# Kernel tuning notes

Measured on AMD Instinct MI355X. Metric: run time of the kernel, lower is better.

## Reference

```python
import jax, jax.numpy as jnp
import numpy as np

EPS = 0.01
MAX_ITER = 100


def setup_inputs() -> dict:
    key = jax.random.key(0)
    B, N = 8, 2048
    c = jax.random.normal(key, (B, N, N), dtype=jnp.float32)
    return {"c": c}


def reference(c):
    # Torch code sets C = -c, then M = (-C + u_i + v_j)/eps = (c + u_i + v_j)/eps.
    eps = EPS
    B, n, _ = c.shape
    log_mu = -jnp.log(jnp.asarray(n, c.dtype))  # log(1/n); mu == nu == uniform
    u = jnp.zeros((B, n), c.dtype)
    v = jnp.zeros((B, n), c.dtype)

    def M(u, v):
        return (c + u[:, :, None] + v[:, None, :]) / eps  # [B, n, n]

    @jax.checkpoint
    def step(carry, _):
        u, v = carry
        # even iteration: u update
        u = eps * (log_mu - jax.nn.logsumexp(M(u, v), axis=-1)) + u
        # odd iteration: v update (logsumexp over transpose == axis -2), then
        # detach + clamp of huge values to 0, as in the torch code
        v_new = eps * (log_mu - jax.nn.logsumexp(M(u, v), axis=-2)) + v
        v_new = jnp.where(v_new > 9e8, jnp.zeros_like(v_new), v_new)
        v = jax.lax.stop_gradient(v_new)
        return (u, v), None

    # 100 torch iterations alternate u/v -> 50 fused (u,v) steps.
    # (Early-break threshold is 1e-12 and essentially never triggers; we run
    #  the fixed max_iter count.)
    (u, v), _ = jax.lax.scan(step, (u, v), None, length=MAX_ITER // 2)

    pi = jnp.exp(M(u, v))
    return pi, -c, u, v
```

## Files before the change

### kernel.cpp

```cpp
#include <hip/hip_runtime.h>

#define NN 2048
#define BB 8
#define NITER 50
#define RCHUNKS 16
#define ROWS_PER_CHUNK (NN / RCHUNKS)

__device__ __forceinline__ float eps_f()      { return 0.01f; }
__device__ __forceinline__ float inv_eps_f()  { return 100.0f; }
__device__ __forceinline__ float eps_logmu_f(){ return -0.0762461898616f; }

__device__ __forceinline__ void lse_combine(float& m, float& s, float om, float os) {
    float M = fmaxf(m, om);
    s = s * __expf((m - M) * inv_eps_f()) + os * __expf((om - M) * inv_eps_f());
    m = M;
}

__global__ __launch_bounds__(256) void k_init(float* __restrict__ u, float* __restrict__ v) {
    int idx = blockIdx.x * 256 + threadIdx.x;
    if (idx < BB * NN) { u[idx] = 0.0f; v[idx] = 0.0f; }
}

__global__ __launch_bounds__(256) void k_u(const float* __restrict__ c,
                                           const float* __restrict__ v,
                                           float* __restrict__ u) {
    int row = blockIdx.x;
    int b   = row >> 11;
    int t   = threadIdx.x;
    const float4* crow = (const float4*)(c + (size_t)row * NN);
    const float4* vb   = (const float4*)(v + (size_t)b * NN);

    float4 c0 = crow[t];
    float4 c1 = crow[t + 256];
    float4 v0 = vb[t];
    float4 v1 = vb[t + 256];

    float x[8] = { c0.x + v0.x, c0.y + v0.y, c0.z + v0.z, c0.w + v0.w,
                   c1.x + v1.x, c1.y + v1.y, c1.z + v1.z, c1.w + v1.w };

    float m = x[0];
#pragma unroll
    for (int k = 1; k < 8; ++k) m = fmaxf(m, x[k]);
    float s = 0.0f;
#pragma unroll
    for (int k = 0; k < 8; ++k) s += __expf((x[k] - m) * inv_eps_f());

#pragma unroll
    for (int off = 32; off; off >>= 1) {
        float om = __shfl_xor(m, off, 64);
        float os = __shfl_xor(s, off, 64);
        lse_combine(m, s, om, os);
    }
    __shared__ float sm[4], ss[4];
    int wid = t >> 6;
    if ((t & 63) == 0) { sm[wid] = m; ss[wid] = s; }
    __syncthreads();
    if (t == 0) {
#pragma unroll
        for (int w = 1; w < 4; ++w) lse_combine(m, s, sm[w], ss[w]);
        u[row] = eps_logmu_f() - m - eps_f() * __logf(s);
    }
}

__global__ __launch_bounds__(256) void k_v_partial(const float* __restrict__ c,
                                                   const float* __restrict__ u,
                                                   float* __restrict__ pm,
                                                   float* __restrict__ ps) {
    int j     = blockIdx.x * 256 + threadIdx.x;
    int chunk = blockIdx.y;
    int b     = blockIdx.z;
    const float* cb = c + (size_t)b * NN * NN;
    const float* ub = u + (size_t)b * NN;

    int i0 = chunk * ROWS_PER_CHUNK;
    float m = -INFINITY, s = 0.0f;
    for (int i = i0; i < i0 + ROWS_PER_CHUNK; i += 4) {
        float u0 = ub[i], u1 = ub[i + 1], u2 = ub[i + 2], u3 = ub[i + 3];
        float x0 = cb[(size_t)(i + 0) * NN + j] + u0;
        float x1 = cb[(size_t)(i + 1) * NN + j] + u1;
        float x2 = cb[(size_t)(i + 2) * NN + j] + u2;
        float x3 = cb[(size_t)(i + 3) * NN + j] + u3;
        float lm = fmaxf(fmaxf(x0, x1), fmaxf(x2, x3));
        float ls = __expf((x0 - lm) * inv_eps_f()) + __expf((x1 - lm) * inv_eps_f())
                 + __expf((x2 - lm) * inv_eps_f()) + __expf((x3 - lm) * inv_eps_f());
        lse_combine(m, s, lm, ls);
    }
    int o = (b * RCHUNKS + chunk) * NN + j;
    pm[o] = m;
    ps[o] = s;
}

__global__ __launch_bounds__(256) void k_v_combine(const float* __restrict__ pm,
                                                   const float* __restrict__ ps,
                                                   float* __restrict__ v) {
    int idx = blockIdx.x * 256 + threadIdx.x;
    int b = idx >> 11;
    int j = idx & (NN - 1);
    float m = -INFINITY, s = 0.0f;
#pragma unroll
    for (int r = 0; r < RCHUNKS; ++r) {
        int o = (b * RCHUNKS + r) * NN + j;
        lse_combine(m, s, pm[o], ps[o]);
    }
    float val = eps_logmu_f() - m - eps_f() * __logf(s);
    if (val > 9e8f) val = 0.0f;
    v[idx] = val;
}

__global__ __launch_bounds__(256) void k_final(const float* __restrict__ c,
                                               const float* __restrict__ u,
                                               const float* __restrict__ v,
                                               float* __restrict__ pi,
                                               float* __restrict__ negc) {
    unsigned q = blockIdx.x * 256 + threadIdx.x;
    unsigned e = q * 4;
    unsigned b = e >> 22;
    unsigned rem = e & (NN * NN - 1);
    unsigned i = rem >> 11;
    unsigned j = rem & (NN - 1);

    float4 cc = ((const float4*)c)[q];
    float ui = u[b * NN + i];
    const float* vp = v + b * NN + j;
    float4 vv = *(const float4*)vp;

    float4 p;
    p.x = __expf((cc.x + ui + vv.x) * inv_eps_f());
    p.y = __expf((cc.y + ui + vv.y) * inv_eps_f());
    p.z = __expf((cc.z + ui + vv.z) * inv_eps_f());
    p.w = __expf((cc.w + ui + vv.w) * inv_eps_f());
    ((float4*)pi)[q] = p;

    float4 nc = { -cc.x, -cc.y, -cc.z, -cc.w };
    ((float4*)negc)[q] = nc;
}

__global__ __launch_bounds__(256) void k_uv_out(const float* __restrict__ u,
                                                const float* __restrict__ v,
                                                float* __restrict__ ou,
                                                float* __restrict__ ov) {
    int idx = blockIdx.x * 256 + threadIdx.x;
    if (idx < BB * NN) { ou[idx] = u[idx]; ov[idx] = v[idx]; }
}

extern "C" void kernel_launch(void* const* d_in, const int* in_sizes, int n_in,
                              void* d_out, int out_size, void* d_ws, size_t ws_size,
                              hipStream_t stream) {
    const float* c = (const float*)d_in[0];
    float* out  = (float*)d_out;
    float* pi   = out;
    float* negc = out + (size_t)BB * NN * NN;
    float* ou   = out + 2 * (size_t)BB * NN * NN;
    float* ov   = ou + BB * NN;

    float* ws = (float*)d_ws;
    float* u  = ws;
    float* v  = ws + BB * NN;
    float* pm = ws + 2 * BB * NN;
    float* ps = pm + BB * RCHUNKS * NN;

    k_init<<<(BB * NN) / 256, 256, 0, stream>>>(u, v);

    dim3 gB(NN / 256, RCHUNKS, BB);
    for (int it = 0; it < NITER; ++it) {
        k_u<<<BB * NN, 256, 0, stream>>>(c, v, u);
        k_v_partial<<<gB, 256, 0, stream>>>(c, u, pm, ps);
        k_v_combine<<<(BB * NN) / 256, 256, 0, stream>>>(pm, ps, v);
    }

    unsigned n4 = (unsigned)((size_t)BB * NN * NN / 4);
    k_final<<<n4 / 256, 256, 0, stream>>>(c, u, v, pi, negc);
    k_uv_out<<<(BB * NN) / 256, 256, 0, stream>>>(u, v, ou, ov);
}
```

Before: 2.563 ms.

## Fuse u-update and partial column logsumexp into one pass over c

Merges the row logsumexp (u update) and the column partial logsumexp (v partials) into a single kernel. Each wave loads a row of c once, computes u for that row, then folds the same registers into per-column running max/sum accumulators. This halves the reads of the 128 MB cost matrix per iteration. In exchange it uses only 512 blocks with heavy register and LDS use, and the v combine step now reads 64 partial bands instead of 16.

```diff
diff --git a/kernel.cpp b/kernel.cpp
--- a/kernel.cpp
+++ b/kernel.cpp
@@ -3,8 +3,9 @@
 #define NN 2048
 #define BB 8
 #define NITER 50
-#define RCHUNKS 16
-#define ROWS_PER_CHUNK (NN / RCHUNKS)
+#define NBAND 64
+#define ROWS_PER_WAVE 8
+#define WPB 4
 
 __device__ __forceinline__ float eps_f()      { return 0.01f; }
 __device__ __forceinline__ float inv_eps_f()  { return 100.0f; }
@@ -16,78 +17,107 @@
     m = M;
 }
 
-__global__ __launch_bounds__(256) void k_init(float* __restrict__ u, float* __restrict__ v) {
+__device__ __forceinline__ void colacc(float& m, float& s, float x) {
+    float M = fmaxf(m, x);
+    s = s * __expf((m - M) * inv_eps_f()) + __expf((x - M) * inv_eps_f());
+    m = M;
+}
+
+__global__ __launch_bounds__(256) void k_init(float* __restrict__ v) {
     int idx = blockIdx.x * 256 + threadIdx.x;
-    if (idx < BB * NN) { u[idx] = 0.0f; v[idx] = 0.0f; }
-}
-
-__global__ __launch_bounds__(256) void k_u(const float* __restrict__ c,
-                                           const float* __restrict__ v,
-                                           float* __restrict__ u) {
-    int row = blockIdx.x;
-    int b   = row >> 11;
-    int t   = threadIdx.x;
-    const float4* crow = (const float4*)(c + (size_t)row * NN);
-    const float4* vb   = (const float4*)(v + (size_t)b * NN);
-
-    float4 c0 = crow[t];
-    float4 c1 = crow[t + 256];
-    float4 v0 = vb[t];
-    float4 v1 = vb[t + 256];
-
-    float x[8] = { c0.x + v0.x, c0.y + v0.y, c0.z + v0.z, c0.w + v0.w,
-                   c1.x + v1.x, c1.y + v1.y, c1.z + v1.z, c1.w + v1.w };
-
-    float m = x[0];
-#pragma unroll
-    for (int k = 1; k < 8; ++k) m = fmaxf(m, x[k]);
-    float s = 0.0f;
-#pragma unroll
-    for (int k = 0; k < 8; ++k) s += __expf((x[k] - m) * inv_eps_f());
-
-#pragma unroll
-    for (int off = 32; off; off >>= 1) {
-        float om = __shfl_xor(m, off, 64);
-        float os = __shfl_xor(s, off, 64);
-        lse_combine(m, s, om, os);
-    }
-    __shared__ float sm[4], ss[4];
-    int wid = t >> 6;
-    if ((t & 63) == 0) { sm[wid] = m; ss[wid] = s; }
+    if (idx < BB * NN) v[idx] = 0.0f;
+}
+
+__global__ __launch_bounds__(256, 2) void k_iter(const float* __restrict__ c,
+                                                 const float* __restrict__ v,
+                                                 float* __restrict__ u,
+                                                 float* __restrict__ pm,
+                                                 float* __restrict__ ps) {
+    __shared__ float lds_v[NN];
+    __shared__ float lds_m[WPB][NN];
+    __shared__ float lds_s[WPB][NN];
+
+    int b    = blockIdx.x >> 6;
+    int band = blockIdx.x & 63;
+    int t    = threadIdx.x;
+    int wave = t >> 6;
+    int lane = t & 63;
+
+    const float4* vg = (const float4*)(v + b * NN);
+    ((float4*)lds_v)[t]       = vg[t];
+    ((float4*)lds_v)[t + 256] = vg[t + 256];
     __syncthreads();
-    if (t == 0) {
-#pragma unroll
-        for (int w = 1; w < 4; ++w) lse_combine(m, s, sm[w], ss[w]);
-        u[row] = eps_logmu_f() - m - eps_f() * __logf(s);
-    }
-}
-
-__global__ __launch_bounds__(256) void k_v_partial(const float* __restrict__ c,
-                                                   const float* __restrict__ u,
-                                                   float* __restrict__ pm,
-                                                   float* __restrict__ ps) {
-    int j     = blockIdx.x * 256 + threadIdx.x;
-    int chunk = blockIdx.y;
-    int b     = blockIdx.z;
-    const float* cb = c + (size_t)b * NN * NN;
-    const float* ub = u + (size_t)b * NN;
-
-    int i0 = chunk * ROWS_PER_CHUNK;
-    float m = -INFINITY, s = 0.0f;
-    for (int i = i0; i < i0 + ROWS_PER_CHUNK; i += 4) {
-        float u0 = ub[i], u1 = ub[i + 1], u2 = ub[i + 2], u3 = ub[i + 3];
-        float x0 = cb[(size_t)(i + 0) * NN + j] + u0;
-        float x1 = cb[(size_t)(i + 1) * NN + j] + u1;
-        float x2 = cb[(size_t)(i + 2) * NN + j] + u2;
-        float x3 = cb[(size_t)(i + 3) * NN + j] + u3;
-        float lm = fmaxf(fmaxf(x0, x1), fmaxf(x2, x3));
-        float ls = __expf((x0 - lm) * inv_eps_f()) + __expf((x1 - lm) * inv_eps_f())
-                 + __expf((x2 - lm) * inv_eps_f()) + __expf((x3 - lm) * inv_eps_f());
-        lse_combine(m, s, lm, ls);
-    }
-    int o = (b * RCHUNKS + chunk) * NN + j;
-    pm[o] = m;
-    ps[o] = s;
+
+    float4 vv[8];
+#pragma unroll
+    for (int q = 0; q < 8; ++q) vv[q] = *(const float4*)(lds_v + q * 256 + lane * 4);
+
+    float4 cm[8], cs[8];
+#pragma unroll
+    for (int q = 0; q < 8; ++q) {
+        cm[q] = make_float4(-INFINITY, -INFINITY, -INFINITY, -INFINITY);
+        cs[q] = make_float4(0.f, 0.f, 0.f, 0.f);
+    }
+
+    int row0 = band * (WPB * ROWS_PER_WAVE) + wave * ROWS_PER_WAVE;
+    const float* cb = c + ((size_t)b * NN + row0) * NN;
+
+    for (int r = 0; r < ROWS_PER_WAVE; ++r) {
+        const float4* crow = (const float4*)(cb + (size_t)r * NN);
+        float4 cr[8];
+#pragma unroll
+        for (int q = 0; q < 8; ++q) cr[q] = crow[q * 64 + lane];
+
+        float m = -INFINITY, s = 0.0f;
+#pragma unroll
+        for (int q = 0; q < 8; ++q) {
+            float x0 = cr[q].x + vv[q].x;
+            float x1 = cr[q].y + vv[q].y;
+            float x2 = cr[q].z + vv[q].z;
+            float x3 = cr[q].w + vv[q].w;
+            float lm = fmaxf(fmaxf(x0, x1), fmaxf(x2, x3));
+            float M  = fmaxf(m, lm);
+            s = s * __expf((m - M) * inv_eps_f())
+              + __expf((x0 - M) * inv_eps_f()) + __expf((x1 - M) * inv_eps_f())
+              + __expf((x2 - M) * inv_eps_f()) + __expf((x3 - M) * inv_eps_f());
+            m = M;
+        }
+#pragma unroll
+        for (int off = 32; off; off >>= 1) {
+            float om = __shfl_xor(m, off, 64);
+            float os = __shfl_xor(s, off, 64);
+            lse_combine(m, s, om, os);
+        }
+        float ui = eps_logmu_f() - m - eps_f() * __logf(s);
+        if (lane == 0) u[b * NN + row0 + r] = ui;
+
+#pragma unroll
+        for (int q = 0; q < 8; ++q) {
+            colacc(cm[q].x, cs[q].x, cr[q].x + ui);
+            colacc(cm[q].y, cs[q].y, cr[q].y + ui);
+            colacc(cm[q].z, cs[q].z, cr[q].z + ui);
+            colacc(cm[q].w, cs[q].w, cr[q].w + ui);
+        }
+    }
+
+#pragma unroll
+    for (int q = 0; q < 8; ++q) {
+        int col = q * 256 + lane * 4;
+        *(float4*)(&lds_m[wave][col]) = cm[q];
+        *(float4*)(&lds_s[wave][col]) = cs[q];
+    }
+    __syncthreads();
+
+    size_t obase = (size_t)(b * NBAND + band) * NN;
+#pragma unroll
+    for (int k = 0; k < 8; ++k) {
+        int col = k * 256 + t;
+        float m = lds_m[0][col], s = lds_s[0][col];
+#pragma unroll
+        for (int w = 1; w < WPB; ++w) lse_combine(m, s, lds_m[w][col], lds_s[w][col]);
+        pm[obase + col] = m;
+        ps[obase + col] = s;
+    }
 }
 
 __global__ __launch_bounds__(256) void k_v_combine(const float* __restrict__ pm,
@@ -97,9 +127,8 @@
     int b = idx >> 11;
     int j = idx & (NN - 1);
     float m = -INFINITY, s = 0.0f;
-#pragma unroll
-    for (int r = 0; r < RCHUNKS; ++r) {
-        int o = (b * RCHUNKS + r) * NN + j;
+    for (int r = 0; r < NBAND; ++r) {
+        size_t o = (size_t)(b * NBAND + r) * NN + j;
         lse_combine(m, s, pm[o], ps[o]);
     }
     float val = eps_logmu_f() - m - eps_f() * __logf(s);
@@ -121,8 +150,7 @@
 
     float4 cc = ((const float4*)c)[q];
     float ui = u[b * NN + i];
-    const float* vp = v + b * NN + j;
-    float4 vv = *(const float4*)vp;
+    float4 vv = *(const float4*)(v + b * NN + j);
 
     float4 p;
     p.x = __expf((cc.x + ui + vv.x) * inv_eps_f());
@@ -157,14 +185,12 @@
     float* u  = ws;
     float* v  = ws + BB * NN;
     float* pm = ws + 2 * BB * NN;
-    float* ps = pm + BB * RCHUNKS * NN;
-
-    k_init<<<(BB * NN) / 256, 256, 0, stream>>>(u, v);
-
-    dim3 gB(NN / 256, RCHUNKS, BB);
+    float* ps = pm + (size_t)BB * NBAND * NN;
+
+    k_init<<<(BB * NN) / 256, 256, 0, stream>>>(v);
+
     for (int it = 0; it < NITER; ++it) {
-        k_u<<<BB * NN, 256, 0, stream>>>(c, v, u);
-        k_v_partial<<<gB, 256, 0, stream>>>(c, u, pm, ps);
+        k_iter<<<BB * NBAND, 256, 0, stream>>>(c, v, u, pm, ps);
         k_v_combine<<<(BB * NN) / 256, 256, 0, stream>>>(pm, ps, v);
     }
 
```

Result: slower. 2.642 ms (+3.1%).
